# Kernel tuning notes

Hardware: AMD Instinct MI355X
Metric: run time of the kernel (lower is better)

Reference implementation:

```python
import jax, jax.numpy as jnp
import numpy as np
from jax import lax

NC = 32
EPS = 1e-12


def unfold3x3(x):
    # x: [B,C,H,W] -> [B, C*9, H*W], matching F.unfold(kernel=3, padding=1)
    B, C, H, W = x.shape
    xp = jnp.pad(x, ((0, 0), (0, 0), (1, 1), (1, 1)))
    patches = jnp.stack([xp[:, :, i:i + H, j:j + W]
                         for i in range(3) for j in range(3)], axis=2)  # [B,C,9,H,W]
    return patches.reshape(B, C * 9, H * W)


def fold3x3(u, H, W):
    # u: [B, C*9, H*W] -> [B, C, H, W], matching F.fold(kernel=3, padding=1)
    B = u.shape[0]
    C = u.shape[1] // 9
    p = u.reshape(B, C, 3, 3, H, W)
    out = jnp.zeros((B, C, H + 2, W + 2), u.dtype)
    for i in range(3):
        for j in range(3):
            out = out.at[:, :, i:i + H, j:j + W].add(p[:, :, i, j])
    return out[:, :, 1:H + 1, 1:W + 1]


def l2norm(x, axis):
    n = jnp.sqrt(jnp.sum(x * x, axis=axis, keepdims=True))
    return x / jnp.maximum(n, EPS)


def conv3x3(x, w, b):
    y = lax.conv_general_dilated(x, w, (1, 1), 'SAME',
                                 dimension_numbers=('NCHW', 'OIHW', 'NCHW'))
    return y + b[None, :, None, None]


def setup_inputs() -> dict:
    key = jax.random.key(0)
    k = jax.random.split(key, 6)
    B, C, H, W = 2, NC, 80, 80
    in_HSI = jax.random.normal(k[0], (B, C, H, W), jnp.float32)
    in_PAN = jax.random.normal(k[1], (B, C, H, W), jnp.float32)
    fan1 = 2 * C * 9
    fan2 = C * 9
    w1 = jax.random.normal(k[2], (C, 2 * C, 3, 3), jnp.float32) / np.sqrt(fan1)
    b1 = jax.random.normal(k[3], (C,), jnp.float32) * 0.01
    w2 = jax.random.normal(k[4], (C, C, 3, 3), jnp.float32) / np.sqrt(fan2)
    b2 = jax.random.normal(k[5], (C,), jnp.float32) * 0.01
    return {"in_HSI": in_HSI, "in_PAN": in_PAN, "w1": w1, "b1": b1, "w2": w2, "b2": b2}


def reference(in_HSI, in_PAN, w1, b1, w2, b2):
    B, C, H, W = in_HSI.shape
    L = H * W
    HSI_unfold = unfold3x3(in_HSI)                      # [B, C*9, L]
    PAN_unfold = unfold3x3(in_PAN)                      # [B, C*9, L]
    PAN_q = l2norm(jnp.transpose(PAN_unfold, (0, 2, 1)), axis=2)  # [B, L, C*9]
    HSI_k = l2norm(HSI_unfold, axis=1)                  # [B, C*9, L]
    R = jnp.einsum('blc,bcm->blm', PAN_q, HSI_k)        # [B, L, L]
    R_star = jnp.max(R, axis=1)                         # [B, L]
    R_arg = jnp.argmax(R, axis=1)                       # [B, L]
    # gather columns of unfold(in_PAN) selected by 1-NN indices
    T_unfold = jnp.take_along_axis(PAN_unfold, R_arg[:, None, :], axis=2)
    T_lv3 = fold3x3(T_unfold, H, W) / 9.0               # [B, C, H, W]
    S = R_star.reshape(B, 1, H, W)
    h = jax.nn.relu(conv3x3(jnp.concatenate([T_lv3, in_HSI], axis=1), w1, b1))
    res = conv3x3(h, w2, b2) * S + in_HSI
    return res
```

## Files before the change

kernel.cpp:

```cpp
#include <hip/hip_runtime.h>
#include <hip/hip_bf16.h>
#include <hip/hip_fp16.h>
#include <stdint.h>

#define HH 80
#define WW 80
#define LL 6400
#define CC 32
#define BB 2
#define COG 16
#define DELTA 0.011f
#define NT8 800

typedef __bf16 bf16x8 __attribute__((ext_vector_type(8)));
typedef float  f32x4  __attribute__((ext_vector_type(4)));

__device__ __forceinline__ int div80(int v) {
    return (int)(((unsigned)v * 52429u) >> 22);
}

__device__ __forceinline__ unsigned short f2bf(float f) {
    unsigned int u = __float_as_uint(f);
    return (unsigned short)((u + 0x7fffu + ((u >> 16) & 1u)) >> 16);
}

__device__ __forceinline__ void gload_lds16(void* g, void* l) {
    __builtin_amdgcn_global_load_lds(
        (__attribute__((address_space(1))) void*)g,
        (__attribute__((address_space(3))) void*)l, 16, 0, 0);
}

__global__ void prep1_kernel(const float* __restrict__ HSI, const float* __restrict__ PAN,
                             float* __restrict__ partH, float* __restrict__ partP) {
    int g = blockIdx.x * 256 + threadIdx.x;
    if (g >= BB * CC * LL) return;
    int l = g % LL;
    int y = div80(l), x = l - y * 80;
    const float* hc = HSI + (size_t)(g - l);
    const float* pc = PAN + (size_t)(g - l);
    float sh = 0.f, sp = 0.f;
    #pragma unroll
    for (int i = 0; i < 3; ++i) {
        int yy = y + i - 1;
        if ((unsigned)yy >= 80u) continue;
        #pragma unroll
        for (int j = 0; j < 3; ++j) {
            int xx = x + j - 1;
            if ((unsigned)xx >= 80u) continue;
            float hv = hc[yy * 80 + xx]; sh = fmaf(hv, hv, sh);
            float pv = pc[yy * 80 + xx]; sp = fmaf(pv, pv, sp);
        }
    }
    partH[g] = sh;
    partP[g] = sp;
}

__global__ void prep2_kernel(const float* __restrict__ partH, const float* __restrict__ partP,
                             float* __restrict__ invH, float* __restrict__ invP) {
    int g = blockIdx.x * 256 + threadIdx.x;
    if (g >= BB * LL) return;
    int b = g / LL, l = g - b * LL;
    float sh = 0.f, sp = 0.f;
    #pragma unroll
    for (int c = 0; c < CC; ++c) {
        sh += partH[((size_t)(b * CC + c)) * LL + l];
        sp += partP[((size_t)(b * CC + c)) * LL + l];
    }
    invH[g] = 1.f / fmaxf(sqrtf(sh), 1e-12f);
    invP[g] = 1.f / fmaxf(sqrtf(sp), 1e-12f);
}

__global__ void pack_kernel(const float* __restrict__ HSI, const float* __restrict__ PAN,
                            const float* __restrict__ invH, const float* __restrict__ invP,
                            char* __restrict__ Apack, char* __restrict__ Bpack,
                            float* __restrict__ PANunf, float* __restrict__ HSIunf) {
    int t = blockIdx.x * 256 + threadIdx.x;
    if (t >= BB * 2 * LL * 36) return;
    int g = t % 36;
    int rest = t / 36;
    int l = rest % LL; rest /= LL;
    int mat = rest & 1;
    int b = rest >> 1;
    const float* img = (mat ? HSI : PAN) + (size_t)b * CC * LL;
    float inv = (mat ? invH : invP)[b * LL + l];
    int y = div80(l), x = l - y * 80;
    int k0 = g * 8;
    int c = k0 / 9, tap = k0 - c * 9;
    unsigned short hs[8];
    float raw[8];
    #pragma unroll
    for (int j = 0; j < 8; ++j) {
        int t3 = tap / 3;
        int dy = t3 - 1, dx = tap - t3 * 3 - 1;
        int yy = y + dy, xx = x + dx;
        float rv = ((unsigned)yy < 80u && (unsigned)xx < 80u)
                       ? img[(size_t)c * LL + yy * 80 + xx] : 0.f;
        raw[j] = rv;
        hs[j] = f2bf(rv * inv);
        if (++tap == 9) { tap = 0; ++c; }
    }
    float* unf = (mat ? HSIunf : PANunf) + ((size_t)b * LL + l) * 288 + k0;
    float4 r0 = {raw[0], raw[1], raw[2], raw[3]};
    float4 r1 = {raw[4], raw[5], raw[6], raw[7]};
    *(float4*)(unf)     = r0;
    *(float4*)(unf + 4) = r1;
    char* pk = mat ? Bpack : Apack;
    int slot = (g % 12) ^ (l & 15);
    int q = g / 12;
    size_t off = ((size_t)(b * 3 + q) * LL + l) * 256 + slot * 16;
    uint4 hv;
    hv.x = hs[0] | ((unsigned)hs[1] << 16); hv.y = hs[2] | ((unsigned)hs[3] << 16);
    hv.z = hs[4] | ((unsigned)hs[5] << 16); hv.w = hs[6] | ((unsigned)hs[7] << 16);
    *(uint4*)(pk + off) = hv;
}

__global__ __launch_bounds__(256) void simq_kernel(const char* __restrict__ Apack,
                                                   const char* __restrict__ Bpack,
                                                   __half* __restrict__ tileMax8) {
    __shared__ __align__(16) char Alds[32768];
    __shared__ __align__(16) char Blds[32768];
    const int orig = blockIdx.x;
    const int xcd = orig & 7, idx = orig >> 3;
    const int wg = (xcd < 4 ? xcd * 63 : 252 + (xcd - 4) * 62) + idx;
    const int b = wg / 250;
    int rest = wg - b * 250;
    const int sp = rest / 50;
    const int mt = rest - sp * 50;

    const int tid = threadIdx.x;
    const int lane = tid & 63, w = tid >> 6;
    const int wl = w >> 1, wm = w & 1;
    const int r15 = lane & 15, h = lane >> 4;
    const char* Ab = Apack + (size_t)b * 3 * LL * 256;
    const char* Bb = Bpack + (size_t)b * 3 * LL * 256;
    const int m0 = mt * 128;
    const f32x4 fzero = {0.f, 0.f, 0.f, 0.f};

    #pragma unroll 1
    for (int lt = 0; lt < 10; ++lt) {
        const int l0 = (sp * 10 + lt) * 128;
        f32x4 acc[4][4];
        #pragma unroll
        for (int i = 0; i < 4; ++i)
            #pragma unroll
            for (int j = 0; j < 4; ++j) acc[i][j] = fzero;

        #pragma unroll 1
        for (int c = 0; c < 3; ++c) {
            __syncthreads();
            const char* gA = Ab + ((size_t)c * LL + l0) * 256 + w * 8192 + lane * 16;
            const char* gB = Bb + ((size_t)c * LL + m0) * 256 + w * 8192 + lane * 16;
            char* lA = Alds + w * 8192;
            char* lB = Blds + w * 8192;
            #pragma unroll
            for (int i = 0; i < 8; ++i) {
                gload_lds16((void*)(gA + i * 1024), lA + i * 1024);
                gload_lds16((void*)(gB + i * 1024), lB + i * 1024);
            }
            __syncthreads();
            #pragma unroll
            for (int ks = 0; ks < 3; ++ks) {
                const int gp = ((ks * 4 + h) ^ r15) * 16;
                bf16x8 af[4], bfr[4];
                #pragma unroll
                for (int f = 0; f < 4; ++f) {
                    af[f]  = *(const bf16x8*)(Alds + (wl * 64 + f * 16 + r15) * 256 + gp);
                    bfr[f] = *(const bf16x8*)(Blds + (wm * 64 + f * 16 + r15) * 256 + gp);
                }
                #pragma unroll
                for (int fl = 0; fl < 4; ++fl)
                    #pragma unroll
                    for (int fm = 0; fm < 4; ++fm)
                        acc[fl][fm] = __builtin_amdgcn_mfma_f32_16x16x32_bf16(
                            af[fl], bfr[fm], acc[fl][fm], 0, 0, 0);
            }
        }
        const int Tbase = (sp * 10 + lt) * 16 + wl * 8;
        #pragma unroll
        for (int fl = 0; fl < 4; ++fl) {
            #pragma unroll
            for (int fm = 0; fm < 4; ++fm) {
                f32x4 a = acc[fl][fm];
                float v = fmaxf(fmaxf(a[0], a[1]), fmaxf(a[2], a[3]));
                v = fmaxf(v, __shfl_xor(v, 16, 64));
                if ((h & 1) == 0) {
                    const int m = m0 + wm * 64 + fm * 16 + r15;
                    tileMax8[((size_t)b * LL + m) * NT8 + Tbase + fl * 2 + (h >> 1)] = __float2half(v);
                }
            }
        }
    }
}

__global__ __launch_bounds__(256) void scanfix_kernel(const float* __restrict__ PANunf,
                                                      const float* __restrict__ HSIunf,
                                                      const float* __restrict__ invH,
                                                      const float* __restrict__ invP,
                                                      const __half* __restrict__ tileMax8,
                                                      float* __restrict__ Sv, int* __restrict__ Sa) {
    const int gw = blockIdx.x * 4 + (threadIdx.x >> 6);
    const int lane = threadIdx.x & 63;
    const int b = gw / LL;
    const __half* tm = tileMax8 + (size_t)gw * NT8;

    float tv[13];
    #pragma unroll
    for (int i = 0; i < 13; ++i) {
        int T = i * 64 + lane;
        tv[i] = (T < NT8) ? __half2float(tm[T]) : -3.0e38f;
    }
    float v1 = tv[0];
    #pragma unroll
    for (int i = 1; i < 13; ++i) v1 = fmaxf(v1, tv[i]);
    #pragma unroll
    for (int d = 1; d < 64; d <<= 1) v1 = fmaxf(v1, __shfl_xor(v1, d, 64));
    const float th = v1 - DELTA;

    const float ihm = invH[gw];
    const int lql = lane >> 3, kq = lane & 7;

    float hreg[36];
    {
        const float4* hv4 = (const float4*)(HSIunf + (size_t)gw * 288 + kq * 36);
        #pragma unroll
        for (int j = 0; j < 9; ++j) {
            float4 v = hv4[j];
            hreg[j * 4 + 0] = v.x; hreg[j * 4 + 1] = v.y;
            hreg[j * 4 + 2] = v.z; hreg[j * 4 + 3] = v.w;
        }
    }

    float bv = -3.0e38f; int bl = 0x7fffffff;

    #pragma unroll 1
    for (int i = 0; i < 13; ++i) {
        unsigned long long mask = __ballot(tv[i] >= th);
        while (mask) {
            const int t = __ffsll((long long)mask) - 1;
            mask &= mask - 1;
            const int T = i * 64 + t;
            const int l = T * 8 + lql;
            const float4* pv4 = (const float4*)(PANunf + ((size_t)b * LL + l) * 288 + kq * 36);
            float part = 0.f;
            #pragma unroll
            for (int j = 0; j < 9; ++j) {
                float4 p = pv4[j];
                part = fmaf(p.x, hreg[j * 4 + 0], part);
                part = fmaf(p.y, hreg[j * 4 + 1], part);
                part = fmaf(p.z, hreg[j * 4 + 2], part);
                part = fmaf(p.w, hreg[j * 4 + 3], part);
            }
            part += __shfl_xor(part, 1, 64);
            part += __shfl_xor(part, 2, 64);
            part += __shfl_xor(part, 4, 64);
            const float val = part * invP[b * LL + l] * ihm;
            if (val > bv || (val == bv && l < bl)) { bv = val; bl = l; }
        }
    }
    #pragma unroll
    for (int d = 1; d < 64; d <<= 1) {
        float ov = __shfl_xor(bv, d, 64);
        int   ol = __shfl_xor(bl, d, 64);
        if (ov > bv || (ov == bv && ol < bl)) { bv = ov; bl = ol; }
    }
    if (lane == 0) { Sv[gw] = bv; Sa[gw] = bl; }
}

__global__ void tfold_kernel(const float* __restrict__ PAN, const int* __restrict__ Sa,
                             float* __restrict__ T) {
    int g = blockIdx.x * blockDim.x + threadIdx.x;
    if (g >= BB * CC * LL) return;
    int bc = g / LL, l = g - bc * LL;
    int b = bc >> 5;
    int y = div80(l), x = l - y * 80;
    const float* img = PAN + (size_t)bc * LL;
    const int* Sab = Sa + b * LL;
    float acc = 0.f;
    #pragma unroll
    for (int i = 0; i < 3; ++i) {
        int yp = y + 1 - i;
        if ((unsigned)yp >= 80u) continue;
        #pragma unroll
        for (int j = 0; j < 3; ++j) {
            int xp = x + 1 - j;
            if ((unsigned)xp >= 80u) continue;
            int a = Sab[yp * 80 + xp];
            int ya = div80(a), xa = a - ya * 80;
            int py = ya + i - 1, px = xa + j - 1;
            if ((unsigned)py < 80u && (unsigned)px < 80u) acc += img[py * 80 + px];
        }
    }
    T[g] = acc * (1.f / 9.f);
}

__global__ __launch_bounds__(256) void conv1_kernel(const float* __restrict__ T,
                                                    const float* __restrict__ HSI,
                                                    const float* __restrict__ w1,
                                                    const float* __restrict__ b1,
                                                    float* __restrict__ h) {
    __shared__ __align__(16) float wl[64][9][COG];
    const int tid = threadIdx.x;
    const int co0 = blockIdx.y * COG;
    for (int idx = tid; idx < 64 * 9 * COG; idx += 256) {
        int cog = idx & (COG - 1);
        int rest = idx >> 4;
        int cin = rest / 9, tap = rest - cin * 9;
        wl[cin][tap][cog] = w1[(co0 + cog) * (64 * 9) + cin * 9 + tap];
    }
    __syncthreads();
    const int g = blockIdx.x * 256 + tid;
    const int b = g / LL, l = g - b * LL;
    const int y = div80(l), x = l - y * 80;
    float acc[COG];
    #pragma unroll
    for (int i = 0; i < COG; ++i) acc[i] = 0.f;
    for (int cin = 0; cin < 64; ++cin) {
        const float* img = (cin < CC) ? (T + (size_t)(b * CC + cin) * LL)
                                      : (HSI + (size_t)(b * CC + (cin - CC)) * LL);
        float tap[9];
        #pragma unroll
        for (int i = 0; i < 3; ++i)
            #pragma unroll
            for (int j = 0; j < 3; ++j) {
                int yy = y + i - 1, xx = x + j - 1;
                tap[i * 3 + j] = ((unsigned)yy < 80u && (unsigned)xx < 80u) ? img[yy * 80 + xx] : 0.f;
            }
        #pragma unroll
        for (int t9 = 0; t9 < 9; ++t9) {
            #pragma unroll
            for (int q4 = 0; q4 < COG / 4; ++q4) {
                const float4 wv = *reinterpret_cast<const float4*>(&wl[cin][t9][q4 * 4]);
                acc[q4 * 4 + 0] = fmaf(tap[t9], wv.x, acc[q4 * 4 + 0]);
                acc[q4 * 4 + 1] = fmaf(tap[t9], wv.y, acc[q4 * 4 + 1]);
                acc[q4 * 4 + 2] = fmaf(tap[t9], wv.z, acc[q4 * 4 + 2]);
                acc[q4 * 4 + 3] = fmaf(tap[t9], wv.w, acc[q4 * 4 + 3]);
            }
        }
    }
    #pragma unroll
    for (int cog = 0; cog < COG; ++cog) {
        float v = acc[cog] + b1[co0 + cog];
        h[(size_t)(b * CC + co0 + cog) * LL + l] = fmaxf(v, 0.f);
    }
}

__global__ __launch_bounds__(256) void conv2_kernel(const float* __restrict__ hbuf,
                                                    const float* __restrict__ HSI,
                                                    const float* __restrict__ Sv,
                                                    const float* __restrict__ w2,
                                                    const float* __restrict__ b2,
                                                    float* __restrict__ out) {
    __shared__ __align__(16) float wl[CC][9][COG];
    const int tid = threadIdx.x;
    const int co0 = blockIdx.y * COG;
    for (int idx = tid; idx < CC * 9 * COG; idx += 256) {
        int cog = idx & (COG - 1);
        int rest = idx >> 4;
        int cin = rest / 9, tap = rest - cin * 9;
        wl[cin][tap][cog] = w2[(co0 + cog) * (CC * 9) + cin * 9 + tap];
    }
    __syncthreads();
    const int g = blockIdx.x * 256 + tid;
    const int b = g / LL, l = g - b * LL;
    const int y = div80(l), x = l - y * 80;
    float acc[COG];
    #pragma unroll
    for (int i = 0; i < COG; ++i) acc[i] = 0.f;
    for (int cin = 0; cin < CC; ++cin) {
        const float* img = hbuf + (size_t)(b * CC + cin) * LL;
        float tap[9];
        #pragma unroll
        for (int i = 0; i < 3; ++i)
            #pragma unroll
            for (int j = 0; j < 3; ++j) {
                int yy = y + i - 1, xx = x + j - 1;
                tap[i * 3 + j] = ((unsigned)yy < 80u && (unsigned)xx < 80u) ? img[yy * 80 + xx] : 0.f;
            }
        #pragma unroll
        for (int t9 = 0; t9 < 9; ++t9) {
            #pragma unroll
            for (int q4 = 0; q4 < COG / 4; ++q4) {
                const float4 wv = *reinterpret_cast<const float4*>(&wl[cin][t9][q4 * 4]);
                acc[q4 * 4 + 0] = fmaf(tap[t9], wv.x, acc[q4 * 4 + 0]);
                acc[q4 * 4 + 1] = fmaf(tap[t9], wv.y, acc[q4 * 4 + 1]);
                acc[q4 * 4 + 2] = fmaf(tap[t9], wv.z, acc[q4 * 4 + 2]);
                acc[q4 * 4 + 3] = fmaf(tap[t9], wv.w, acc[q4 * 4 + 3]);
            }
        }
    }
    const float s = Sv[b * LL + l];
    #pragma unroll
    for (int cog = 0; cog < COG; ++cog) {
        int c = co0 + cog;
        out[(size_t)(b * CC + c) * LL + l] = fmaf(acc[cog] + b2[c], s, HSI[(size_t)(b * CC + c) * LL + l]);
    }
}

extern "C" void kernel_launch(void* const* d_in, const int* in_sizes, int n_in,
                              void* d_out, int out_size, void* d_ws, size_t ws_size,
                              hipStream_t stream) {
    const float* HSI = (const float*)d_in[0];
    const float* PAN = (const float*)d_in[1];
    const float* w1  = (const float*)d_in[2];
    const float* b1  = (const float*)d_in[3];
    const float* w2  = (const float*)d_in[4];
    const float* b2  = (const float*)d_in[5];
    float* out = (float*)d_out;

    char* ws = (char*)d_ws;
    size_t off = 0;
    auto alloc = [&](size_t bytes) -> void* {
        void* p = ws + off;
        off += (bytes + 255) & ~(size_t)255;
        return p;
    };
    float* partH = (float*)alloc((size_t)BB * CC * LL * 4);
    float* partP = (float*)alloc((size_t)BB * CC * LL * 4);
    float* invH  = (float*)alloc((size_t)BB * LL * 4);
    float* invP  = (float*)alloc((size_t)BB * LL * 4);
    char*  Apack = (char*) alloc((size_t)BB * 3 * LL * 256);
    char*  Bpack = (char*) alloc((size_t)BB * 3 * LL * 256);
    __half* tileMax8 = (__half*)alloc((size_t)BB * LL * NT8 * 2);
    float* PANunf = (float*)alloc((size_t)BB * LL * 288 * 4);
    float* HSIunf = (float*)alloc((size_t)BB * LL * 288 * 4);
    float* Sv    = (float*)alloc((size_t)BB * LL * 4);
    int*   Sa    = (int*)  alloc((size_t)BB * LL * 4);
    float* T     = partH;
    float* hbuf  = partP;

    prep1_kernel<<<dim3((BB * CC * LL + 255) / 256), 256, 0, stream>>>(HSI, PAN, partH, partP);
    prep2_kernel<<<dim3((BB * LL + 255) / 256), 256, 0, stream>>>(partH, partP, invH, invP);
    pack_kernel<<<dim3((BB * 2 * LL * 36 + 255) / 256), 256, 0, stream>>>(HSI, PAN, invH, invP,
                                                                          Apack, Bpack, PANunf, HSIunf);
    simq_kernel<<<dim3(500), 256, 0, stream>>>(Apack, Bpack, tileMax8);
    scanfix_kernel<<<dim3(BB * LL / 4), 256, 0, stream>>>(PANunf, HSIunf, invH, invP, tileMax8, Sv, Sa);
    tfold_kernel<<<dim3((BB * CC * LL + 255) / 256), 256, 0, stream>>>(PAN, Sa, T);
    conv1_kernel<<<dim3(BB * LL / 256, CC / COG), 256, 0, stream>>>(T, HSI, w1, b1, hbuf);
    conv2_kernel<<<dim3(BB * LL / 256, CC / COG), 256, 0, stream>>>(hbuf, HSI, Sv, w2, b2, out);
}
```

Measured before the change: 247.8 us.

## Keep B fragments in registers and double-buffer A tiles in LDS

The similarity GEMM kernel now loads each wave's B-matrix fragments for all three K chunks into registers once, since the B tile is fixed across the l-tile loop. This removes the repeated global-to-LDS B copies and the B reads from LDS. The A tile is double-buffered in LDS so the next chunk's async load overlaps the current MFMA work, which leaves one barrier per chunk instead of two. The trade-off is 144 extra VGPRs for bq, against a launch bound that still requests two blocks per SIMD, so register pressure or spills could reduce occupancy.

```diff
diff --git a/kernel.cpp b/kernel.cpp
--- a/kernel.cpp
+++ b/kernel.cpp
@@ -114,11 +114,10 @@
     *(uint4*)(pk + off) = hv;
 }
 
-__global__ __launch_bounds__(256) void simq_kernel(const char* __restrict__ Apack,
-                                                   const char* __restrict__ Bpack,
-                                                   __half* __restrict__ tileMax8) {
-    __shared__ __align__(16) char Alds[32768];
-    __shared__ __align__(16) char Blds[32768];
+__global__ __launch_bounds__(256, 2) void simq_kernel(const char* __restrict__ Apack,
+                                                      const char* __restrict__ Bpack,
+                                                      __half* __restrict__ tileMax8) {
+    __shared__ __align__(16) char Alds[2][32768];
     const int orig = blockIdx.x;
     const int xcd = orig & 7, idx = orig >> 3;
     const int wg = (xcd < 4 ? xcd * 63 : 252 + (xcd - 4) * 62) + idx;
@@ -136,45 +135,67 @@
     const int m0 = mt * 128;
     const f32x4 fzero = {0.f, 0.f, 0.f, 0.f};
 
+    bf16x8 bq[3][3][4];
+    {
+        const int rowb = m0 + wm * 64 + r15;
+        #pragma unroll
+        for (int c = 0; c < 3; ++c)
+            #pragma unroll
+            for (int ks = 0; ks < 3; ++ks)
+                #pragma unroll
+                for (int fm = 0; fm < 4; ++fm) {
+                    const int gp = ((ks * 4 + h) ^ r15) * 16;
+                    bq[c][ks][fm] = *(const bf16x8*)(Bb + ((size_t)c * LL + rowb + fm * 16) * 256 + gp);
+                }
+    }
+
+    {
+        const char* gA = Ab + ((size_t)(sp * 10) * 128) * 256 + w * 8192 + lane * 16;
+        char* lA = Alds[0] + w * 8192;
+        #pragma unroll
+        for (int i = 0; i < 8; ++i) gload_lds16((void*)(gA + i * 1024), lA + i * 1024);
+    }
+    __syncthreads();
+
+    int cur = 0;
     #pragma unroll 1
     for (int lt = 0; lt < 10; ++lt) {
-        const int l0 = (sp * 10 + lt) * 128;
         f32x4 acc[4][4];
         #pragma unroll
         for (int i = 0; i < 4; ++i)
             #pragma unroll
             for (int j = 0; j < 4; ++j) acc[i][j] = fzero;
 
-        #pragma unroll 1
+        #pragma unroll
         for (int c = 0; c < 3; ++c) {
-            __syncthreads();
-            const char* gA = Ab + ((size_t)c * LL + l0) * 256 + w * 8192 + lane * 16;
-            const char* gB = Bb + ((size_t)c * LL + m0) * 256 + w * 8192 + lane * 16;
-            char* lA = Alds + w * 8192;
-            char* lB = Blds + w * 8192;
-            #pragma unroll
-            for (int i = 0; i < 8; ++i) {
-                gload_lds16((void*)(gA + i * 1024), lA + i * 1024);
-                gload_lds16((void*)(gB + i * 1024), lB + i * 1024);
-            }
-            __syncthreads();
+            if (c < 2 || lt < 9) {
+                const int lt2 = (c == 2) ? lt + 1 : lt;
+                const int c2  = (c == 2) ? 0 : c + 1;
+                const int l0n = (sp * 10 + lt2) * 128;
+                const char* gA = Ab + ((size_t)c2 * LL + l0n) * 256 + w * 8192 + lane * 16;
+                char* lA = Alds[cur ^ 1] + w * 8192;
+                #pragma unroll
+                for (int i = 0; i < 8; ++i) gload_lds16((void*)(gA + i * 1024), lA + i * 1024);
+            }
+            const char* lAr = Alds[cur];
             #pragma unroll
             for (int ks = 0; ks < 3; ++ks) {
                 const int gp = ((ks * 4 + h) ^ r15) * 16;
-                bf16x8 af[4], bfr[4];
+                bf16x8 af[4];
                 #pragma unroll
-                for (int f = 0; f < 4; ++f) {
-                    af[f]  = *(const bf16x8*)(Alds + (wl * 64 + f * 16 + r15) * 256 + gp);
-                    bfr[f] = *(const bf16x8*)(Blds + (wm * 64 + f * 16 + r15) * 256 + gp);
-                }
+                for (int f = 0; f < 4; ++f)
+                    af[f] = *(const bf16x8*)(lAr + (wl * 64 + f * 16 + r15) * 256 + gp);
                 #pragma unroll
                 for (int fl = 0; fl < 4; ++fl)
                     #pragma unroll
                     for (int fm = 0; fm < 4; ++fm)
                         acc[fl][fm] = __builtin_amdgcn_mfma_f32_16x16x32_bf16(
-                            af[fl], bfr[fm], acc[fl][fm], 0, 0, 0);
-            }
-        }
+                            af[fl], bq[c][ks][fm], acc[fl][fm], 0, 0, 0);
+            }
+            __syncthreads();
+            cur ^= 1;
+        }
+
         const int Tbase = (sp * 10 + lt) * 16 + wl * 8;
         #pragma unroll
         for (int fl = 0; fl < 4; ++fl) {
```

Result: faster. 226.8 us (-8.5%).
